# Optimization experiments

Measured on AMD Instinct MI355X. Metric: run time of the kernel, lower is better.

## Reference

```python
import jax, jax.numpy as jnp
import numpy as np

N_NODES = 100000
N_EDGES = 3200000
NUM_FEATURES = 128
DIM = 10
NUM_GRAPHS = 64


def setup_inputs() -> dict:
    key = jax.random.key(0)
    k1, k2, k3, k4, k5, k6, k7 = jax.random.split(key, 7)
    features = jax.random.normal(k1, (N_NODES, NUM_FEATURES), dtype=jnp.float32)
    src = jax.random.randint(k2, (N_EDGES,), 0, N_NODES, dtype=jnp.int64)
    dst = jax.random.randint(k3, (N_EDGES,), 0, N_NODES, dtype=jnp.int64)
    graph_ids = jnp.sort(jax.random.randint(k4, (N_NODES,), 0, NUM_GRAPHS, dtype=jnp.int64))
    # GraphConv weights (no bias), glorot-ish scaling
    W1 = jax.random.normal(k5, (NUM_FEATURES, DIM), dtype=jnp.float32) / np.sqrt(NUM_FEATURES)
    W2 = jax.random.normal(k6, (DIM, DIM), dtype=jnp.float32) / np.sqrt(DIM)
    W3 = jax.random.normal(k7, (DIM, 1), dtype=jnp.float32) / np.sqrt(DIM)
    return {"features": features, "W1": W1, "W2": W2, "W3": W3,
            "src": src, "dst": dst, "graph_ids": graph_ids}


def _sum_aggregate(h, src, dst, n_nodes):
    # message = h[src], reduce-sum at dst (norm='none' GraphConv aggregation)
    return jax.ops.segment_sum(h[src], dst, num_segments=n_nodes)


def reference(features, W1, W2, W3, src, dst, graph_ids):
    n = features.shape[0]
    # conv1: in_feats(128) > out_feats(10) -> weight first, then aggregate
    h = features @ W1                          # [N, DIM]
    h = _sum_aggregate(h, src, dst, n)         # [N, DIM]
    h = jax.nn.relu(h)
    # conv2: in_feats == out_feats -> aggregate first, then weight
    h = _sum_aggregate(h, src, dst, n) @ W2    # [N, DIM]
    # dgl.mean_nodes: per-graph mean pooling over nodes
    sums = jax.ops.segment_sum(h, graph_ids, num_segments=NUM_GRAPHS)           # [G, DIM]
    cnt = jax.ops.segment_sum(jnp.ones((n, 1), h.dtype), graph_ids, num_segments=NUM_GRAPHS)
    pooled = sums / jnp.maximum(cnt, 1.0)      # [G, DIM]
    return jax.nn.sigmoid(pooled @ W3)         # [G, 1]
```

## Files before the change

### kernel.cpp

```cpp
#include <hip/hip_runtime.h>
#include <hip/hip_fp16.h>

#define N_NODES 100000
#define N_EDGES 3200000
#define NUM_FEATURES 128
#define DIM 10
#define NUM_GRAPHS 64

#define BSHIFT 8
#define BSIZE (1 << BSHIFT)
#define NB ((N_NODES + BSIZE - 1) / BSIZE)
#define CHUNKS 4
#define PCHUNKS 4
#define EPB 12500
#define PLACE_BLOCKS 256
#define NQUAD 25000
#define GEMM_BLOCKS 1563
#define BOUND_BLOCKS 196
#define TILE (BSIZE * DIM)
#define CAP 2560
#define CAPB 16384
#define NCHUNK (NB * CHUNKS)
#define NCHUNK2 (NB * PCHUNKS)
#define ACC_STRIDE 11

#define DPP_ROR_ADD(v, n)                                                        \
    (v) += __int_as_float(__builtin_amdgcn_update_dpp(                           \
        0, __float_as_int(v), 0x120 | (n), 0xF, 0xF, false))

__global__ __launch_bounds__(512, 2) void k_front(const float* __restrict__ feat,
                                                  const float* __restrict__ W1,
                                                  __half* __restrict__ h1,
                                                  const int* __restrict__ gids,
                                                  int* __restrict__ bound,
                                                  const int* __restrict__ src,
                                                  const int* __restrict__ dst,
                                                  int* __restrict__ cnt,
                                                  int* __restrict__ pk) {
    __shared__ int hd[NB];
    __shared__ int cb[NB];

    if (blockIdx.x < PLACE_BLOCKS) {
        int base0 = blockIdx.x * EPB;
        for (int t = threadIdx.x; t < NB; t += 512) hd[t] = 0;
        __syncthreads();

        {
            int i = threadIdx.x;
            for (; i + 1536 < EPB; i += 2048) {
                int d0 = dst[base0 + i],        d1 = dst[base0 + i + 512];
                int d2 = dst[base0 + i + 1024], d3 = dst[base0 + i + 1536];
                atomicAdd(&hd[d0 >> BSHIFT], 1);
                atomicAdd(&hd[d1 >> BSHIFT], 1);
                atomicAdd(&hd[d2 >> BSHIFT], 1);
                atomicAdd(&hd[d3 >> BSHIFT], 1);
            }
            for (; i < EPB; i += 512)
                atomicAdd(&hd[dst[base0 + i] >> BSHIFT], 1);
        }
        __syncthreads();

        for (int t = threadIdx.x; t < NB; t += 512) {
            int c = hd[t];
            int o = c ? atomicAdd(&cnt[t], c) : 0;
            cb[t] = t * CAPB + o;
        }
        __syncthreads();

        {
            int i = threadIdx.x;
            for (; i + 1536 < EPB; i += 2048) {
                int d0 = dst[base0 + i],        d1 = dst[base0 + i + 512];
                int d2 = dst[base0 + i + 1024], d3 = dst[base0 + i + 1536];
                int s0 = src[base0 + i],        s1 = src[base0 + i + 512];
                int s2 = src[base0 + i + 1024], s3 = src[base0 + i + 1536];
                int q0 = atomicAdd(&cb[d0 >> BSHIFT], 1);
                int q1 = atomicAdd(&cb[d1 >> BSHIFT], 1);
                int q2 = atomicAdd(&cb[d2 >> BSHIFT], 1);
                int q3 = atomicAdd(&cb[d3 >> BSHIFT], 1);
                if (q0 < ((d0 >> BSHIFT) + 1) * CAPB) pk[q0] = ((d0 & (BSIZE - 1)) << 17) | s0;
                if (q1 < ((d1 >> BSHIFT) + 1) * CAPB) pk[q1] = ((d1 & (BSIZE - 1)) << 17) | s1;
                if (q2 < ((d2 >> BSHIFT) + 1) * CAPB) pk[q2] = ((d2 & (BSIZE - 1)) << 17) | s2;
                if (q3 < ((d3 >> BSHIFT) + 1) * CAPB) pk[q3] = ((d3 & (BSIZE - 1)) << 17) | s3;
            }
            for (; i < EPB; i += 512) {
                int d = dst[base0 + i];
                int s = src[base0 + i];
                int q = atomicAdd(&cb[d >> BSHIFT], 1);
                if (q < ((d >> BSHIFT) + 1) * CAPB) pk[q] = ((d & (BSIZE - 1)) << 17) | s;
            }
        }
        return;
    }

    int bb = blockIdx.x - PLACE_BLOCKS;

    int nb2 = bb * 512 + threadIdx.x;
    if (bb < BOUND_BLOCKS && nb2 < N_NODES) {
        int g  = gids[nb2];
        int gp = nb2 ? gids[nb2 - 1] : -1;
        for (int v = gp + 1; v <= g; ++v) bound[v] = nb2;
        if (nb2 == N_NODES - 1)
            for (int v = g + 1; v <= NUM_GRAPHS; ++v) bound[v] = N_NODES;
    }

    int gid  = bb * 512 + threadIdx.x;
    int quad = gid >> 5;
    int lane = gid & 31;
    if (quad >= NQUAD) return;

    float wf[40];
    {
        const float4* W14 = reinterpret_cast<const float4*>(W1 + lane * 40);
#pragma unroll
        for (int m = 0; m < 10; ++m) {
            float4 q = W14[m];
            wf[4 * m]     = q.x;
            wf[4 * m + 1] = q.y;
            wf[4 * m + 2] = q.z;
            wf[4 * m + 3] = q.w;
        }
    }

    int nbase = quad * 4;
    float4 f[4];
#pragma unroll
    for (int n = 0; n < 4; ++n)
        f[n] = *reinterpret_cast<const float4*>(feat + (size_t)(nbase + n) * NUM_FEATURES + lane * 4);

    float acc[4][DIM];
#pragma unroll
    for (int n = 0; n < 4; ++n)
#pragma unroll
        for (int k = 0; k < DIM; ++k) acc[n][k] = 0.f;

#pragma unroll
    for (int n = 0; n < 4; ++n) {
        float fv[4] = {f[n].x, f[n].y, f[n].z, f[n].w};
#pragma unroll
        for (int j = 0; j < 4; ++j)
#pragma unroll
            for (int k = 0; k < DIM; ++k)
                acc[n][k] += fv[j] * wf[j * DIM + k];
    }

#pragma unroll
    for (int n = 0; n < 4; ++n)
#pragma unroll
        for (int k = 0; k < DIM; ++k) {
            float v = acc[n][k];
            DPP_ROR_ADD(v, 1);
            DPP_ROR_ADD(v, 2);
            DPP_ROR_ADD(v, 4);
            DPP_ROR_ADD(v, 8);
            acc[n][k] = v + __shfl_xor(v, 16);
        }

    if (lane == 0) {
        __half2* o = (__half2*)h1;
#pragma unroll
        for (int n = 0; n < 4; ++n)
#pragma unroll
            for (int j = 0; j < 5; ++j)
                o[(size_t)(nbase + n) * 5 + j] =
                    __floats2half2_rn(acc[n][2 * j], acc[n][2 * j + 1]);
    }
}

__global__ __launch_bounds__(512) void k_spmm1(const __half* __restrict__ h,
                                               const int* __restrict__ cnt,
                                               const int* __restrict__ pk,
                                               float* __restrict__ part) {
    __shared__ int eh[CAP];
    __shared__ int srt[CAP];
    __shared__ int hist[BSIZE];
    __shared__ int cur[BSIZE];

    int b     = blockIdx.x / CHUNKS;
    int chunk = blockIdx.x % CHUNKS;
    int s0  = b * CAPB;
    int len = cnt[b];
    int c0  = s0 + (len * chunk) / CHUNKS;
    int c1  = s0 + (len * (chunk + 1)) / CHUNKS;
    int n   = c1 - c0;
    int nc  = min(n, CAP);

    for (int t = threadIdx.x; t < BSIZE; t += 512) hist[t] = 0;
    __syncthreads();

    {
        int i = threadIdx.x;
        for (; i + 1536 < nc; i += 2048) {
            int p0 = pk[c0 + i],        p1 = pk[c0 + i + 512];
            int p2 = pk[c0 + i + 1024], p3 = pk[c0 + i + 1536];
            eh[i] = p0; eh[i + 512] = p1; eh[i + 1024] = p2; eh[i + 1536] = p3;
            atomicAdd(&hist[p0 >> 17], 1);
            atomicAdd(&hist[p1 >> 17], 1);
            atomicAdd(&hist[p2 >> 17], 1);
            atomicAdd(&hist[p3 >> 17], 1);
        }
        for (; i < nc; i += 512) {
            int p = pk[c0 + i];
            eh[i] = p;
            atomicAdd(&hist[p >> 17], 1);
        }
    }
    __syncthreads();

    if (threadIdx.x < 64) {
        int l = threadIdx.x;
        int carry = 0;
#pragma unroll
        for (int j = 0; j < 4; ++j) {
            int x = hist[j * 64 + l];
            int v = x;
#pragma unroll
            for (int off = 1; off < 64; off <<= 1) {
                int t2 = __shfl_up(v, off);
                if (l >= off) v += t2;
            }
            cur[j * 64 + l] = carry + v - x;
            carry += __shfl(v, 63);
        }
    }
    __syncthreads();

    for (int i = threadIdx.x; i < nc; i += 512) {
        int p = eh[i];
        int pos = atomicAdd(&cur[p >> 17], 1);
        srt[pos] = p;
    }
    __syncthreads();

    int wave = threadIdx.x >> 6;
    int lane = threadIdx.x & 63;
    int slot = lane / 5;
    int l    = lane - slot * 5;
    float* pb = part + (size_t)blockIdx.x * TILE;
    const __half2* h2 = (const __half2*)h;

    if (slot < 12) {
        int g = wave * 12 + slot;
        for (int loc = g; loc < BSIZE; loc += 96) {
            int e0 = loc ? cur[loc - 1] : 0;
            int e1 = cur[loc];
            float ax0 = 0.f, ay0 = 0.f, ax1 = 0.f, ay1 = 0.f;
            float ax2 = 0.f, ay2 = 0.f, ax3 = 0.f, ay3 = 0.f;
            int e = e0;
            for (; e + 7 < e1; e += 8) {
                float2 v0 = __half22float2(h2[(size_t)(srt[e]     & 0x1FFFF) * 5 + l]);
                float2 v1 = __half22float2(h2[(size_t)(srt[e + 1] & 0x1FFFF) * 5 + l]);
                float2 v2 = __half22float2(h2[(size_t)(srt[e + 2] & 0x1FFFF) * 5 + l]);
                float2 v3 = __half22float2(h2[(size_t)(srt[e + 3] & 0x1FFFF) * 5 + l]);
                float2 v4 = __half22float2(h2[(size_t)(srt[e + 4] & 0x1FFFF) * 5 + l]);
                float2 v5 = __half22float2(h2[(size_t)(srt[e + 5] & 0x1FFFF) * 5 + l]);
                float2 v6 = __half22float2(h2[(size_t)(srt[e + 6] & 0x1FFFF) * 5 + l]);
                float2 v7 = __half22float2(h2[(size_t)(srt[e + 7] & 0x1FFFF) * 5 + l]);
                ax0 += v0.x + v4.x; ay0 += v0.y + v4.y;
                ax1 += v1.x + v5.x; ay1 += v1.y + v5.y;
                ax2 += v2.x + v6.x; ay2 += v2.y + v6.y;
                ax3 += v3.x + v7.x; ay3 += v3.y + v7.y;
            }
            for (; e < e1; ++e) {
                float2 v = __half22float2(h2[(size_t)(srt[e] & 0x1FFFF) * 5 + l]);
                ax0 += v.x; ay0 += v.y;
            }
            pb[loc * DIM + 2 * l]     = (ax0 + ax1) + (ax2 + ax3);
            pb[loc * DIM + 2 * l + 1] = (ay0 + ay1) + (ay2 + ay3);
        }
    }
    __syncthreads();

    for (int i = CAP + threadIdx.x; i < n; i += 512) {
        int p = pk[c0 + i];
        int loc = p >> 17, s = p & 0x1FFFF;
#pragma unroll
        for (int j = 0; j < 5; ++j) {
            float2 v = __half22float2(h2[(size_t)s * 5 + j]);
            atomicAdd(&pb[loc * DIM + 2 * j], v.x);
            atomicAdd(&pb[loc * DIM + 2 * j + 1], v.y);
        }
    }
}

__global__ __launch_bounds__(256) void k_merge_relu(const float* __restrict__ part,
                                                    __half* __restrict__ r) {
    int b     = blockIdx.x;
    int nbase = b << BSHIFT;
    const float* p0 = part + (size_t)(b * CHUNKS) * TILE;
    __half2* r2 = (__half2*)r;
    for (int t = threadIdx.x; t < TILE / 2; t += 256) {
        float sx = 0.f, sy = 0.f;
#pragma unroll
        for (int c = 0; c < CHUNKS; ++c) {
            float2 v = ((const float2*)(p0 + (size_t)c * TILE))[t];
            sx += v.x; sy += v.y;
        }
        int ebase = nbase * DIM + 2 * t;
        if (ebase < N_NODES * DIM)
            r2[(size_t)nbase * 5 + t] = __floats2half2_rn(fmaxf(sx, 0.f), fmaxf(sy, 0.f));
    }
}

__global__ __launch_bounds__(512) void k_pass2(const __half* __restrict__ r,
                                               const int* __restrict__ cnt,
                                               const int* __restrict__ pk,
                                               const int* __restrict__ bound,
                                               float* __restrict__ sums) {
    __shared__ float acc[NUM_GRAPHS * ACC_STRIDE];

    int b     = blockIdx.x / PCHUNKS;
    int chunk = blockIdx.x % PCHUNKS;
    int nbase = b << BSHIFT;
    int nlast = min(nbase + BSIZE - 1, N_NODES - 1);

    int glo = 0, ghx = NUM_GRAPHS - 1;
#pragma unroll
    for (int it = 0; it < 6; ++it) {
        int mid = (glo + ghx + 1) >> 1;
        if (bound[mid] <= nbase) glo = mid; else ghx = mid - 1;
    }
    int lo2 = 0, hi2 = NUM_GRAPHS - 1;
#pragma unroll
    for (int it = 0; it < 6; ++it) {
        int mid = (lo2 + hi2 + 1) >> 1;
        if (bound[mid] <= nlast) lo2 = mid; else hi2 = mid - 1;
    }
    int ghi  = lo2;
    int span = ghi - glo;

    for (int t = threadIdx.x; t < (span + 1) * DIM; t += 512)
        acc[(glo + t / DIM) * ACC_STRIDE + t % DIM] = 0.f;
    __syncthreads();

    int s0  = b * CAPB;
    int len = cnt[b];
    int c0  = s0 + (len * chunk) / PCHUNKS;
    int c1  = s0 + (len * (chunk + 1)) / PCHUNKS;

    int wave = threadIdx.x >> 6;
    int lane = threadIdx.x & 63;
    int slot = lane / 5;
    int l    = lane - slot * 5;
    const __half2* r2 = (const __half2*)r;

    if (slot < 12) {
        const int STR = 96;
        int q = wave * 12 + slot;
        int e = c0 + q;
        if (span <= 1) {
            int gA  = glo;
            int gB  = (span == 1) ? glo + 1 : glo;
            int cut = (span == 1) ? (bound[glo + 1] - nbase) : BSIZE;
            float axA = 0.f, ayA = 0.f, axB = 0.f, ayB = 0.f;
            for (; e + 7 * STR < c1; e += 8 * STR) {
                int p[8];
#pragma unroll
                for (int u = 0; u < 8; ++u) p[u] = pk[e + u * STR];
                float2 v[8];
#pragma unroll
                for (int u = 0; u < 8; ++u)
                    v[u] = __half22float2(r2[(size_t)(p[u] & 0x1FFFF) * 5 + l]);
#pragma unroll
                for (int u = 0; u < 8; ++u) {
                    bool a = (p[u] >> 17) < cut;
                    axA += a ? v[u].x : 0.f;  ayA += a ? v[u].y : 0.f;
                    axB += a ? 0.f : v[u].x;  ayB += a ? 0.f : v[u].y;
                }
            }
            for (; e < c1; e += STR) {
                int p = pk[e];
                float2 v = __half22float2(r2[(size_t)(p & 0x1FFFF) * 5 + l]);
                bool a = (p >> 17) < cut;
                axA += a ? v.x : 0.f;  ayA += a ? v.y : 0.f;
                axB += a ? 0.f : v.x;  ayB += a ? 0.f : v.y;
            }
            atomicAdd(&acc[gA * ACC_STRIDE + 2 * l], axA);
            atomicAdd(&acc[gA * ACC_STRIDE + 2 * l + 1], ayA);
            if (span == 1) {
                atomicAdd(&acc[gB * ACC_STRIDE + 2 * l], axB);
                atomicAdd(&acc[gB * ACC_STRIDE + 2 * l + 1], ayB);
            }
        } else {
            for (; e < c1; e += STR) {
                int p   = pk[e];
                int loc = p >> 17;
                float2 v = __half22float2(r2[(size_t)(p & 0x1FFFF) * 5 + l]);
                int g = glo;
                for (int gg = glo + 1; gg <= ghi; ++gg)
                    g += (loc >= bound[gg] - nbase) ? 1 : 0;
                atomicAdd(&acc[g * ACC_STRIDE + 2 * l], v.x);
                atomicAdd(&acc[g * ACC_STRIDE + 2 * l + 1], v.y);
            }
        }
    }
    __syncthreads();

    for (int t = threadIdx.x; t < (span + 1) * DIM; t += 512) {
        int g = glo + t / DIM;
        float v = acc[g * ACC_STRIDE + t % DIM];
        if (v != 0.f) atomicAdd(&sums[g * DIM + t % DIM], v);
    }
}

__global__ void k_final(const float* __restrict__ sums, const int* __restrict__ bound,
                        const float* __restrict__ W2, const float* __restrict__ W3,
                        float* __restrict__ out) {
    int g = threadIdx.x;
    if (g >= NUM_GRAPHS) return;
    float c = fmaxf((float)(bound[g + 1] - bound[g]), 1.f);
    float p[DIM];
#pragma unroll
    for (int k = 0; k < DIM; ++k) p[k] = sums[g * DIM + k] / c;
    float z = 0.f;
#pragma unroll
    for (int j = 0; j < DIM; ++j) {
        float t = 0.f;
#pragma unroll
        for (int k = 0; k < DIM; ++k) t += p[k] * W2[k * DIM + j];
        z += t * W3[j];
    }
    out[g] = 1.f / (1.f + expf(-z));
}

extern "C" void kernel_launch(void* const* d_in, const int* in_sizes, int n_in,
                              void* d_out, int out_size, void* d_ws, size_t ws_size,
                              hipStream_t stream) {
    const float* feat = (const float*)d_in[0];
    const float* W1   = (const float*)d_in[1];
    const float* W2   = (const float*)d_in[2];
    const float* W3   = (const float*)d_in[3];
    const int*   src  = (const int*)d_in[4];
    const int*   dst  = (const int*)d_in[5];
    const int*   gids = (const int*)d_in[6];
    float*       out  = (float*)d_out;

    char* ws = (char*)d_ws;
    __half* h1    = (__half*)(ws);
    int*    pk    = (int*)(ws + 2000000);
    __half* r     = (__half*)(ws + 27624576);
    float*  part  = (float*)(ws + 29624576);
    int*    cnt   = (int*)(ws + 45639936);
    float*  sums  = (float*)(ws + 45641504);
    int*    bound = (int*)(ws + 45644064);

    hipMemsetAsync(ws + 45639936, 0, 4128, stream);

    k_front<<<PLACE_BLOCKS + GEMM_BLOCKS, 512, 0, stream>>>(feat, W1, h1, gids, bound,
                                                            src, dst, cnt, pk);
    k_spmm1     <<<NCHUNK, 512, 0, stream>>>(h1, cnt, pk, part);
    k_merge_relu<<<NB, 256, 0, stream>>>(part, r);
    k_pass2     <<<NCHUNK2, 512, 0, stream>>>(r, cnt, pk, bound, sums);

    k_final<<<1, 64, 0, stream>>>(sums, bound, W2, W3, out);
}
```

Measured before the change: 206.7 us.

## Pad node feature rows to 32 bytes and gather with float4 loads

Node feature rows of h1 and r are stored in half precision, padded from 10 to 16 halves (32 bytes), so each row can be fetched with two 16-byte float4 loads. The spmm and pooling kernels now map two lanes per destination or edge instead of five, and each lane accumulates 8 values. This cuts the number of gather instructions and raises per-wave parallelism, at the cost of 60% more bytes per row in memory, more registers per lane, and wasted padding lanes. The workspace offsets are shifted to fit the larger buffers, and k_front's occupancy hint in launch_bounds is dropped.

```diff
diff --git a/kernel.cpp b/kernel.cpp
--- a/kernel.cpp
+++ b/kernel.cpp
@@ -23,20 +23,45 @@
 #define NCHUNK (NB * CHUNKS)
 #define NCHUNK2 (NB * PCHUNKS)
 #define ACC_STRIDE 11
+#define ROWH2 8
 
 #define DPP_ROR_ADD(v, n)                                                        \
     (v) += __int_as_float(__builtin_amdgcn_update_dpp(                           \
         0, __float_as_int(v), 0x120 | (n), 0xF, 0xF, false))
 
-__global__ __launch_bounds__(512, 2) void k_front(const float* __restrict__ feat,
-                                                  const float* __restrict__ W1,
-                                                  __half* __restrict__ h1,
-                                                  const int* __restrict__ gids,
-                                                  int* __restrict__ bound,
-                                                  const int* __restrict__ src,
-                                                  const int* __restrict__ dst,
-                                                  int* __restrict__ cnt,
-                                                  int* __restrict__ pk) {
+__device__ __forceinline__ void acc8(const float4& q, float a[8]) {
+    float2 u0 = __half22float2(__builtin_bit_cast(__half2, q.x));
+    float2 u1 = __half22float2(__builtin_bit_cast(__half2, q.y));
+    float2 u2 = __half22float2(__builtin_bit_cast(__half2, q.z));
+    float2 u3 = __half22float2(__builtin_bit_cast(__half2, q.w));
+    a[0] += u0.x; a[1] += u0.y; a[2] += u1.x; a[3] += u1.y;
+    a[4] += u2.x; a[5] += u2.y; a[6] += u3.x; a[7] += u3.y;
+}
+
+__device__ __forceinline__ void selacc8(const float4& q, bool s, float aA[8], float aB[8]) {
+    float2 u0 = __half22float2(__builtin_bit_cast(__half2, q.x));
+    float2 u1 = __half22float2(__builtin_bit_cast(__half2, q.y));
+    float2 u2 = __half22float2(__builtin_bit_cast(__half2, q.z));
+    float2 u3 = __half22float2(__builtin_bit_cast(__half2, q.w));
+    aA[0] += s ? u0.x : 0.f;  aB[0] += s ? 0.f : u0.x;
+    aA[1] += s ? u0.y : 0.f;  aB[1] += s ? 0.f : u0.y;
+    aA[2] += s ? u1.x : 0.f;  aB[2] += s ? 0.f : u1.x;
+    aA[3] += s ? u1.y : 0.f;  aB[3] += s ? 0.f : u1.y;
+    aA[4] += s ? u2.x : 0.f;  aB[4] += s ? 0.f : u2.x;
+    aA[5] += s ? u2.y : 0.f;  aB[5] += s ? 0.f : u2.y;
+    aA[6] += s ? u3.x : 0.f;  aB[6] += s ? 0.f : u3.x;
+    aA[7] += s ? u3.y : 0.f;  aB[7] += s ? 0.f : u3.y;
+}
+
+__global__ __launch_bounds__(512) void k_front(const float* __restrict__ feat,
+                                               const float* __restrict__ W1,
+                                               __half* __restrict__ h1,
+                                               const int* __restrict__ gids,
+                                               int* __restrict__ bound,
+                                               const int* __restrict__ src,
+                                               const int* __restrict__ dst,
+                                               int* __restrict__ cnt,
+                                               int* __restrict__ pk) {
     __shared__ int hd[NB];
     __shared__ int cb[NB];
 
@@ -157,13 +182,19 @@
         }
 
     if (lane == 0) {
-        __half2* o = (__half2*)h1;
-#pragma unroll
-        for (int n = 0; n < 4; ++n)
-#pragma unroll
-            for (int j = 0; j < 5; ++j)
-                o[(size_t)(nbase + n) * 5 + j] =
-                    __floats2half2_rn(acc[n][2 * j], acc[n][2 * j + 1]);
+        float4* o4 = (float4*)h1;
+#pragma unroll
+        for (int n = 0; n < 4; ++n) {
+            float4 w0, w1;
+            w0.x = __builtin_bit_cast(float, __floats2half2_rn(acc[n][0], acc[n][1]));
+            w0.y = __builtin_bit_cast(float, __floats2half2_rn(acc[n][2], acc[n][3]));
+            w0.z = __builtin_bit_cast(float, __floats2half2_rn(acc[n][4], acc[n][5]));
+            w0.w = __builtin_bit_cast(float, __floats2half2_rn(acc[n][6], acc[n][7]));
+            w1.x = __builtin_bit_cast(float, __floats2half2_rn(acc[n][8], acc[n][9]));
+            w1.y = 0.f; w1.z = 0.f; w1.w = 0.f;
+            o4[(size_t)(nbase + n) * 2 + 0] = w0;
+            o4[(size_t)(nbase + n) * 2 + 1] = w1;
+        }
     }
 }
 
@@ -234,49 +265,54 @@
 
     int wave = threadIdx.x >> 6;
     int lane = threadIdx.x & 63;
-    int slot = lane / 5;
-    int l    = lane - slot * 5;
+    int slot = lane >> 1;
+    int l    = lane & 1;
     float* pb = part + (size_t)blockIdx.x * TILE;
-    const __half2* h2 = (const __half2*)h;
-
-    if (slot < 12) {
-        int g = wave * 12 + slot;
-        for (int loc = g; loc < BSIZE; loc += 96) {
-            int e0 = loc ? cur[loc - 1] : 0;
-            int e1 = cur[loc];
-            float ax0 = 0.f, ay0 = 0.f, ax1 = 0.f, ay1 = 0.f;
-            float ax2 = 0.f, ay2 = 0.f, ax3 = 0.f, ay3 = 0.f;
-            int e = e0;
-            for (; e + 7 < e1; e += 8) {
-                float2 v0 = __half22float2(h2[(size_t)(srt[e]     & 0x1FFFF) * 5 + l]);
-                float2 v1 = __half22float2(h2[(size_t)(srt[e + 1] & 0x1FFFF) * 5 + l]);
-                float2 v2 = __half22float2(h2[(size_t)(srt[e + 2] & 0x1FFFF) * 5 + l]);
-                float2 v3 = __half22float2(h2[(size_t)(srt[e + 3] & 0x1FFFF) * 5 + l]);
-                float2 v4 = __half22float2(h2[(size_t)(srt[e + 4] & 0x1FFFF) * 5 + l]);
-                float2 v5 = __half22float2(h2[(size_t)(srt[e + 5] & 0x1FFFF) * 5 + l]);
-                float2 v6 = __half22float2(h2[(size_t)(srt[e + 6] & 0x1FFFF) * 5 + l]);
-                float2 v7 = __half22float2(h2[(size_t)(srt[e + 7] & 0x1FFFF) * 5 + l]);
-                ax0 += v0.x + v4.x; ay0 += v0.y + v4.y;
-                ax1 += v1.x + v5.x; ay1 += v1.y + v5.y;
-                ax2 += v2.x + v6.x; ay2 += v2.y + v6.y;
-                ax3 += v3.x + v7.x; ay3 += v3.y + v7.y;
-            }
-            for (; e < e1; ++e) {
-                float2 v = __half22float2(h2[(size_t)(srt[e] & 0x1FFFF) * 5 + l]);
-                ax0 += v.x; ay0 += v.y;
-            }
-            pb[loc * DIM + 2 * l]     = (ax0 + ax1) + (ax2 + ax3);
-            pb[loc * DIM + 2 * l + 1] = (ay0 + ay1) + (ay2 + ay3);
-        }
-    }
-    __syncthreads();
-
+    const float4* h4 = (const float4*)h;
+
+    {
+        int g  = wave * 32 + slot;
+        int e0 = g ? cur[g - 1] : 0;
+        int e1 = cur[g];
+        float a[8]  = {0.f, 0.f, 0.f, 0.f, 0.f, 0.f, 0.f, 0.f};
+        float b2[8] = {0.f, 0.f, 0.f, 0.f, 0.f, 0.f, 0.f, 0.f};
+        int e = e0;
+        for (; e + 7 < e1; e += 8) {
+            float4 q0 = h4[(size_t)(srt[e]     & 0x1FFFF) * 2 + l];
+            float4 q1 = h4[(size_t)(srt[e + 1] & 0x1FFFF) * 2 + l];
+            float4 q2 = h4[(size_t)(srt[e + 2] & 0x1FFFF) * 2 + l];
+            float4 q3 = h4[(size_t)(srt[e + 3] & 0x1FFFF) * 2 + l];
+            float4 q4 = h4[(size_t)(srt[e + 4] & 0x1FFFF) * 2 + l];
+            float4 q5 = h4[(size_t)(srt[e + 5] & 0x1FFFF) * 2 + l];
+            float4 q6 = h4[(size_t)(srt[e + 6] & 0x1FFFF) * 2 + l];
+            float4 q7 = h4[(size_t)(srt[e + 7] & 0x1FFFF) * 2 + l];
+            acc8(q0, a); acc8(q1, b2); acc8(q2, a); acc8(q3, b2);
+            acc8(q4, a); acc8(q5, b2); acc8(q6, a); acc8(q7, b2);
+        }
+        for (; e < e1; ++e)
+            acc8(h4[(size_t)(srt[e] & 0x1FFFF) * 2 + l], a);
+#pragma unroll
+        for (int j = 0; j < 8; ++j) a[j] += b2[j];
+
+        float2* pb2 = (float2*)pb;
+        if (l == 0) {
+            pb2[g * 5 + 0] = make_float2(a[0], a[1]);
+            pb2[g * 5 + 1] = make_float2(a[2], a[3]);
+            pb2[g * 5 + 2] = make_float2(a[4], a[5]);
+            pb2[g * 5 + 3] = make_float2(a[6], a[7]);
+        } else {
+            pb2[g * 5 + 4] = make_float2(a[0], a[1]);
+        }
+    }
+    __syncthreads();
+
+    const __half2* h2f = (const __half2*)h;
     for (int i = CAP + threadIdx.x; i < n; i += 512) {
         int p = pk[c0 + i];
         int loc = p >> 17, s = p & 0x1FFFF;
 #pragma unroll
         for (int j = 0; j < 5; ++j) {
-            float2 v = __half22float2(h2[(size_t)s * 5 + j]);
+            float2 v = __half22float2(h2f[(size_t)s * ROWH2 + j]);
             atomicAdd(&pb[loc * DIM + 2 * j], v.x);
             atomicAdd(&pb[loc * DIM + 2 * j + 1], v.y);
         }
@@ -289,16 +325,24 @@
     int nbase = b << BSHIFT;
     const float* p0 = part + (size_t)(b * CHUNKS) * TILE;
     __half2* r2 = (__half2*)r;
-    for (int t = threadIdx.x; t < TILE / 2; t += 256) {
-        float sx = 0.f, sy = 0.f;
-#pragma unroll
-        for (int c = 0; c < CHUNKS; ++c) {
-            float2 v = ((const float2*)(p0 + (size_t)c * TILE))[t];
-            sx += v.x; sy += v.y;
-        }
-        int ebase = nbase * DIM + 2 * t;
-        if (ebase < N_NODES * DIM)
-            r2[(size_t)nbase * 5 + t] = __floats2half2_rn(fmaxf(sx, 0.f), fmaxf(sy, 0.f));
+    for (int t = threadIdx.x; t < BSIZE * ROWH2; t += 256) {
+        int node = t >> 3;
+        int j    = t & 7;
+        int gn   = nbase + node;
+        if (gn >= N_NODES) break;
+        __half2 outv;
+        if (j < 5) {
+            float sx = 0.f, sy = 0.f;
+#pragma unroll
+            for (int c = 0; c < CHUNKS; ++c) {
+                float2 v = ((const float2*)(p0 + (size_t)c * TILE))[node * 5 + j];
+                sx += v.x; sy += v.y;
+            }
+            outv = __floats2half2_rn(fmaxf(sx, 0.f), fmaxf(sy, 0.f));
+        } else {
+            outv = __floats2half2_rn(0.f, 0.f);
+        }
+        r2[(size_t)gn * ROWH2 + j] = outv;
     }
 }
 
@@ -340,57 +384,77 @@
 
     int wave = threadIdx.x >> 6;
     int lane = threadIdx.x & 63;
-    int slot = lane / 5;
-    int l    = lane - slot * 5;
-    const __half2* r2 = (const __half2*)r;
-
-    if (slot < 12) {
-        const int STR = 96;
-        int q = wave * 12 + slot;
+    int slot = lane >> 1;
+    int l    = lane & 1;
+    const float4* r4 = (const float4*)r;
+
+    {
+        const int STR = 256;
+        int q = wave * 32 + slot;
         int e = c0 + q;
         if (span <= 1) {
             int gA  = glo;
             int gB  = (span == 1) ? glo + 1 : glo;
             int cut = (span == 1) ? (bound[glo + 1] - nbase) : BSIZE;
-            float axA = 0.f, ayA = 0.f, axB = 0.f, ayB = 0.f;
-            for (; e + 7 * STR < c1; e += 8 * STR) {
-                int p[8];
-#pragma unroll
-                for (int u = 0; u < 8; ++u) p[u] = pk[e + u * STR];
-                float2 v[8];
-#pragma unroll
-                for (int u = 0; u < 8; ++u)
-                    v[u] = __half22float2(r2[(size_t)(p[u] & 0x1FFFF) * 5 + l]);
-#pragma unroll
-                for (int u = 0; u < 8; ++u) {
-                    bool a = (p[u] >> 17) < cut;
-                    axA += a ? v[u].x : 0.f;  ayA += a ? v[u].y : 0.f;
-                    axB += a ? 0.f : v[u].x;  ayB += a ? 0.f : v[u].y;
-                }
+            float aA[8] = {0.f, 0.f, 0.f, 0.f, 0.f, 0.f, 0.f, 0.f};
+            float aB[8] = {0.f, 0.f, 0.f, 0.f, 0.f, 0.f, 0.f, 0.f};
+            for (; e + 3 * STR < c1; e += 4 * STR) {
+                int p0 = pk[e], p1 = pk[e + STR], p2 = pk[e + 2 * STR], p3 = pk[e + 3 * STR];
+                float4 q0 = r4[(size_t)(p0 & 0x1FFFF) * 2 + l];
+                float4 q1 = r4[(size_t)(p1 & 0x1FFFF) * 2 + l];
+                float4 q2 = r4[(size_t)(p2 & 0x1FFFF) * 2 + l];
+                float4 q3 = r4[(size_t)(p3 & 0x1FFFF) * 2 + l];
+                selacc8(q0, (p0 >> 17) < cut, aA, aB);
+                selacc8(q1, (p1 >> 17) < cut, aA, aB);
+                selacc8(q2, (p2 >> 17) < cut, aA, aB);
+                selacc8(q3, (p3 >> 17) < cut, aA, aB);
             }
             for (; e < c1; e += STR) {
                 int p = pk[e];
-                float2 v = __half22float2(r2[(size_t)(p & 0x1FFFF) * 5 + l]);
-                bool a = (p >> 17) < cut;
-                axA += a ? v.x : 0.f;  ayA += a ? v.y : 0.f;
-                axB += a ? 0.f : v.x;  ayB += a ? 0.f : v.y;
-            }
-            atomicAdd(&acc[gA * ACC_STRIDE + 2 * l], axA);
-            atomicAdd(&acc[gA * ACC_STRIDE + 2 * l + 1], ayA);
+                float4 qv = r4[(size_t)(p & 0x1FFFF) * 2 + l];
+                selacc8(qv, (p >> 17) < cut, aA, aB);
+            }
+            if (l == 0) {
+#pragma unroll
+                for (int j = 0; j < 8; ++j) atomicAdd(&acc[gA * ACC_STRIDE + j], aA[j]);
+            } else {
+                atomicAdd(&acc[gA * ACC_STRIDE + 8], aA[0]);
+                atomicAdd(&acc[gA * ACC_STRIDE + 9], aA[1]);
+            }
             if (span == 1) {
-                atomicAdd(&acc[gB * ACC_STRIDE + 2 * l], axB);
-                atomicAdd(&acc[gB * ACC_STRIDE + 2 * l + 1], ayB);
+                if (l == 0) {
+#pragma unroll
+                    for (int j = 0; j < 8; ++j) atomicAdd(&acc[gB * ACC_STRIDE + j], aB[j]);
+                } else {
+                    atomicAdd(&acc[gB * ACC_STRIDE + 8], aB[0]);
+                    atomicAdd(&acc[gB * ACC_STRIDE + 9], aB[1]);
+                }
             }
         } else {
             for (; e < c1; e += STR) {
                 int p   = pk[e];
                 int loc = p >> 17;
-                float2 v = __half22float2(r2[(size_t)(p & 0x1FFFF) * 5 + l]);
+                float4 qv = r4[(size_t)(p & 0x1FFFF) * 2 + l];
+                float2 u0 = __half22float2(__builtin_bit_cast(__half2, qv.x));
+                float2 u1 = __half22float2(__builtin_bit_cast(__half2, qv.y));
+                float2 u2 = __half22float2(__builtin_bit_cast(__half2, qv.z));
+                float2 u3 = __half22float2(__builtin_bit_cast(__half2, qv.w));
                 int g = glo;
                 for (int gg = glo + 1; gg <= ghi; ++gg)
                     g += (loc >= bound[gg] - nbase) ? 1 : 0;
-                atomicAdd(&acc[g * ACC_STRIDE + 2 * l], v.x);
-                atomicAdd(&acc[g * ACC_STRIDE + 2 * l + 1], v.y);
+                if (l == 0) {
+                    atomicAdd(&acc[g * ACC_STRIDE + 0], u0.x);
+                    atomicAdd(&acc[g * ACC_STRIDE + 1], u0.y);
+                    atomicAdd(&acc[g * ACC_STRIDE + 2], u1.x);
+                    atomicAdd(&acc[g * ACC_STRIDE + 3], u1.y);
+                    atomicAdd(&acc[g * ACC_STRIDE + 4], u2.x);
+                    atomicAdd(&acc[g * ACC_STRIDE + 5], u2.y);
+                    atomicAdd(&acc[g * ACC_STRIDE + 6], u3.x);
+                    atomicAdd(&acc[g * ACC_STRIDE + 7], u3.y);
+                } else {
+                    atomicAdd(&acc[g * ACC_STRIDE + 8], u0.x);
+                    atomicAdd(&acc[g * ACC_STRIDE + 9], u0.y);
+                }
             }
         }
     }
@@ -437,14 +501,14 @@
 
     char* ws = (char*)d_ws;
     __half* h1    = (__half*)(ws);
-    int*    pk    = (int*)(ws + 2000000);
-    __half* r     = (__half*)(ws + 27624576);
-    float*  part  = (float*)(ws + 29624576);
-    int*    cnt   = (int*)(ws + 45639936);
-    float*  sums  = (float*)(ws + 45641504);
-    int*    bound = (int*)(ws + 45644064);
-
-    hipMemsetAsync(ws + 45639936, 0, 4128, stream);
+    int*    pk    = (int*)(ws + 3200000);
+    __half* r     = (__half*)(ws + 28824576);
+    float*  part  = (float*)(ws + 32024576);
+    int*    cnt   = (int*)(ws + 48039936);
+    float*  sums  = (float*)(ws + 48041504);
+    int*    bound = (int*)(ws + 48044064);
+
+    hipMemsetAsync(ws + 48039936, 0, 4128, stream);
 
     k_front<<<PLACE_BLOCKS + GEMM_BLOCKS, 512, 0, stream>>>(feat, W1, h1, gids, bound,
                                                             src, dst, cnt, pk);
```

New measurement: 226.4 us. 9.5% more time.

## Drop merge kernel: atomically accumulate conv1 output in fp32, apply relu in pass2

Applied to the files above, without the earlier changes.

The per-chunk partial tiles and the separate merge+relu kernel are removed. spmm1 chunks now atomically add their per-node sums straight into a zeroed fp32 node buffer, and pass2 reads that fp32 buffer and applies relu on load. This saves a kernel launch and the partial-buffer write/read round trip. In exchange it adds global float atomics, a larger memset, and a gather in pass2 that reads fp32 instead of fp16, doubling the bytes per gathered row. The k_front launch bounds also drop the min-blocks hint, which changes its register budget.

```diff
diff --git a/kernel.cpp b/kernel.cpp
--- a/kernel.cpp
+++ b/kernel.cpp
@@ -17,7 +17,6 @@
 #define NQUAD 25000
 #define GEMM_BLOCKS 1563
 #define BOUND_BLOCKS 196
-#define TILE (BSIZE * DIM)
 #define CAP 2560
 #define CAPB 16384
 #define NCHUNK (NB * CHUNKS)
@@ -28,15 +27,15 @@
     (v) += __int_as_float(__builtin_amdgcn_update_dpp(                           \
         0, __float_as_int(v), 0x120 | (n), 0xF, 0xF, false))
 
-__global__ __launch_bounds__(512, 2) void k_front(const float* __restrict__ feat,
-                                                  const float* __restrict__ W1,
-                                                  __half* __restrict__ h1,
-                                                  const int* __restrict__ gids,
-                                                  int* __restrict__ bound,
-                                                  const int* __restrict__ src,
-                                                  const int* __restrict__ dst,
-                                                  int* __restrict__ cnt,
-                                                  int* __restrict__ pk) {
+__global__ __launch_bounds__(512) void k_front(const float* __restrict__ feat,
+                                               const float* __restrict__ W1,
+                                               __half* __restrict__ h1,
+                                               const int* __restrict__ gids,
+                                               int* __restrict__ bound,
+                                               const int* __restrict__ src,
+                                               const int* __restrict__ dst,
+                                               int* __restrict__ cnt,
+                                               int* __restrict__ pk) {
     __shared__ int hd[NB];
     __shared__ int cb[NB];
 
@@ -162,15 +161,14 @@
         for (int n = 0; n < 4; ++n)
 #pragma unroll
             for (int j = 0; j < 5; ++j)
-                o[(size_t)(nbase + n) * 5 + j] =
-                    __floats2half2_rn(acc[n][2 * j], acc[n][2 * j + 1]);
+                o[(size_t)(nbase + n) * 5 + j] = __floats2half2_rn(acc[n][2 * j], acc[n][2 * j + 1]);
     }
 }
 
 __global__ __launch_bounds__(512) void k_spmm1(const __half* __restrict__ h,
                                                const int* __restrict__ cnt,
                                                const int* __restrict__ pk,
-                                               float* __restrict__ part) {
+                                               float* __restrict__ rf32) {
     __shared__ int eh[CAP];
     __shared__ int srt[CAP];
     __shared__ int hist[BSIZE];
@@ -236,7 +234,6 @@
     int lane = threadIdx.x & 63;
     int slot = lane / 5;
     int l    = lane - slot * 5;
-    float* pb = part + (size_t)blockIdx.x * TILE;
     const __half2* h2 = (const __half2*)h;
 
     if (slot < 12) {
@@ -244,6 +241,7 @@
         for (int loc = g; loc < BSIZE; loc += 96) {
             int e0 = loc ? cur[loc - 1] : 0;
             int e1 = cur[loc];
+            if (e1 <= e0) continue;
             float ax0 = 0.f, ay0 = 0.f, ax1 = 0.f, ay1 = 0.f;
             float ax2 = 0.f, ay2 = 0.f, ax3 = 0.f, ay3 = 0.f;
             int e = e0;
@@ -265,8 +263,9 @@
                 float2 v = __half22float2(h2[(size_t)(srt[e] & 0x1FFFF) * 5 + l]);
                 ax0 += v.x; ay0 += v.y;
             }
-            pb[loc * DIM + 2 * l]     = (ax0 + ax1) + (ax2 + ax3);
-            pb[loc * DIM + 2 * l + 1] = (ay0 + ay1) + (ay2 + ay3);
+            int node = (b << BSHIFT) + loc;
+            atomicAdd(&rf32[(size_t)node * DIM + 2 * l],     (ax0 + ax1) + (ax2 + ax3));
+            atomicAdd(&rf32[(size_t)node * DIM + 2 * l + 1], (ay0 + ay1) + (ay2 + ay3));
         }
     }
     __syncthreads();
@@ -274,35 +273,17 @@
     for (int i = CAP + threadIdx.x; i < n; i += 512) {
         int p = pk[c0 + i];
         int loc = p >> 17, s = p & 0x1FFFF;
+        int node = (b << BSHIFT) + loc;
 #pragma unroll
         for (int j = 0; j < 5; ++j) {
             float2 v = __half22float2(h2[(size_t)s * 5 + j]);
-            atomicAdd(&pb[loc * DIM + 2 * j], v.x);
-            atomicAdd(&pb[loc * DIM + 2 * j + 1], v.y);
+            atomicAdd(&rf32[(size_t)node * DIM + 2 * j], v.x);
+            atomicAdd(&rf32[(size_t)node * DIM + 2 * j + 1], v.y);
         }
     }
 }
 
-__global__ __launch_bounds__(256) void k_merge_relu(const float* __restrict__ part,
-                                                    __half* __restrict__ r) {
-    int b     = blockIdx.x;
-    int nbase = b << BSHIFT;
-    const float* p0 = part + (size_t)(b * CHUNKS) * TILE;
-    __half2* r2 = (__half2*)r;
-    for (int t = threadIdx.x; t < TILE / 2; t += 256) {
-        float sx = 0.f, sy = 0.f;
-#pragma unroll
-        for (int c = 0; c < CHUNKS; ++c) {
-            float2 v = ((const float2*)(p0 + (size_t)c * TILE))[t];
-            sx += v.x; sy += v.y;
-        }
-        int ebase = nbase * DIM + 2 * t;
-        if (ebase < N_NODES * DIM)
-            r2[(size_t)nbase * 5 + t] = __floats2half2_rn(fmaxf(sx, 0.f), fmaxf(sy, 0.f));
-    }
-}
-
-__global__ __launch_bounds__(512) void k_pass2(const __half* __restrict__ r,
+__global__ __launch_bounds__(512) void k_pass2(const float* __restrict__ rf32,
                                                const int* __restrict__ cnt,
                                                const int* __restrict__ pk,
                                                const int* __restrict__ bound,
@@ -342,7 +323,7 @@
     int lane = threadIdx.x & 63;
     int slot = lane / 5;
     int l    = lane - slot * 5;
-    const __half2* r2 = (const __half2*)r;
+    const float2* r2 = (const float2*)rf32;
 
     if (slot < 12) {
         const int STR = 96;
@@ -359,8 +340,11 @@
                 for (int u = 0; u < 8; ++u) p[u] = pk[e + u * STR];
                 float2 v[8];
 #pragma unroll
-                for (int u = 0; u < 8; ++u)
-                    v[u] = __half22float2(r2[(size_t)(p[u] & 0x1FFFF) * 5 + l]);
+                for (int u = 0; u < 8; ++u) {
+                    v[u] = r2[(size_t)(p[u] & 0x1FFFF) * 5 + l];
+                    v[u].x = fmaxf(v[u].x, 0.f);
+                    v[u].y = fmaxf(v[u].y, 0.f);
+                }
 #pragma unroll
                 for (int u = 0; u < 8; ++u) {
                     bool a = (p[u] >> 17) < cut;
@@ -370,7 +354,9 @@
             }
             for (; e < c1; e += STR) {
                 int p = pk[e];
-                float2 v = __half22float2(r2[(size_t)(p & 0x1FFFF) * 5 + l]);
+                float2 v = r2[(size_t)(p & 0x1FFFF) * 5 + l];
+                v.x = fmaxf(v.x, 0.f);
+                v.y = fmaxf(v.y, 0.f);
                 bool a = (p >> 17) < cut;
                 axA += a ? v.x : 0.f;  ayA += a ? v.y : 0.f;
                 axB += a ? 0.f : v.x;  ayB += a ? 0.f : v.y;
@@ -385,7 +371,9 @@
             for (; e < c1; e += STR) {
                 int p   = pk[e];
                 int loc = p >> 17;
-                float2 v = __half22float2(r2[(size_t)(p & 0x1FFFF) * 5 + l]);
+                float2 v = r2[(size_t)(p & 0x1FFFF) * 5 + l];
+                v.x = fmaxf(v.x, 0.f);
+                v.y = fmaxf(v.y, 0.f);
                 int g = glo;
                 for (int gg = glo + 1; gg <= ghi; ++gg)
                     g += (loc >= bound[gg] - nbase) ? 1 : 0;
@@ -438,19 +426,17 @@
     char* ws = (char*)d_ws;
     __half* h1    = (__half*)(ws);
     int*    pk    = (int*)(ws + 2000000);
-    __half* r     = (__half*)(ws + 27624576);
-    float*  part  = (float*)(ws + 29624576);
-    int*    cnt   = (int*)(ws + 45639936);
-    float*  sums  = (float*)(ws + 45641504);
-    int*    bound = (int*)(ws + 45644064);
-
-    hipMemsetAsync(ws + 45639936, 0, 4128, stream);
+    float*  rf32  = (float*)(ws + 27624576);
+    int*    cnt   = (int*)(ws + 31624576);
+    float*  sums  = (float*)(ws + 31626144);
+    int*    bound = (int*)(ws + 31628704);
+
+    hipMemsetAsync(ws + 27624576, 0, 4004128, stream);
 
     k_front<<<PLACE_BLOCKS + GEMM_BLOCKS, 512, 0, stream>>>(feat, W1, h1, gids, bound,
                                                             src, dst, cnt, pk);
-    k_spmm1     <<<NCHUNK, 512, 0, stream>>>(h1, cnt, pk, part);
-    k_merge_relu<<<NB, 256, 0, stream>>>(part, r);
-    k_pass2     <<<NCHUNK2, 512, 0, stream>>>(r, cnt, pk, bound, sums);
+    k_spmm1<<<NCHUNK, 512, 0, stream>>>(h1, cnt, pk, rf32);
+    k_pass2<<<NCHUNK2, 512, 0, stream>>>(rf32, cnt, pk, bound, sums);
 
     k_final<<<1, 64, 0, stream>>>(sums, bound, W2, W3, out);
 }
```

New measurement: 218.7 us. +5.8%, slower.
